# Performance work log

Hardware: AMD Instinct MI355X
Metric: run time of the kernel (lower is better)

Reference implementation:

```python
import jax, jax.numpy as jnp
import numpy as np

FEATURES = 1024
NUM_HEADS = 16
HEAD_SIZE = FEATURES // NUM_HEADS
B, T = 4, 2048
LN_EPS = 1e-6


def setup_inputs() -> dict:
    key = jax.random.key(0)
    ks = jax.random.split(key, 12)
    C, H, D = FEATURES, NUM_HEADS, HEAD_SIZE
    s_in = 1.0 / np.sqrt(C)
    s_ff = 1.0 / np.sqrt(4 * C)
    return {
        "x": jax.random.normal(ks[0], (B, T, C), jnp.float32),
        # per-head Q/K/V projections (no bias), stacked over heads
        "wq": jax.random.normal(ks[1], (H, C, D), jnp.float32) * s_in,
        "wk": jax.random.normal(ks[2], (H, C, D), jnp.float32) * s_in,
        "wv": jax.random.normal(ks[3], (H, C, D), jnp.float32) * s_in,
        "w_proj": jax.random.normal(ks[4], (C, C), jnp.float32) * s_in,
        "b_proj": jnp.zeros((C,), jnp.float32),
        "w_ff1": jax.random.normal(ks[5], (C, 4 * C), jnp.float32) * s_in,
        "b_ff1": jnp.zeros((4 * C,), jnp.float32),
        "w_ff2": jax.random.normal(ks[6], (4 * C, C), jnp.float32) * s_ff,
        "b_ff2": jnp.zeros((C,), jnp.float32),
        "ln1_scale": jnp.ones((C,), jnp.float32),
        "ln1_bias": jnp.zeros((C,), jnp.float32),
        "ln2_scale": jnp.ones((C,), jnp.float32),
        "ln2_bias": jnp.zeros((C,), jnp.float32),
    }


def _layernorm(x, scale, bias):
    mu = jnp.mean(x, axis=-1, keepdims=True)
    var = jnp.mean(jnp.square(x - mu), axis=-1, keepdims=True)
    return (x - mu) * jax.lax.rsqrt(var + LN_EPS) * scale + bias


def reference(x, wq, wk, wv, w_proj, b_proj, w_ff1, b_ff1, w_ff2, b_ff2,
              ln1_scale, ln1_bias, ln2_scale, ln2_bias):
    Bn, Tn, C = x.shape
    res = x
    xn = _layernorm(x, ln1_scale, ln1_bias)
    # per-head projections, vectorized over heads: [B,H,T,D]
    q = jnp.einsum('btc,hcd->bhtd', xn, wq)
    k = jnp.einsum('btc,hcd->bhtd', xn, wk)
    v = jnp.einsum('btc,hcd->bhtd', xn, wv)
    wei = jnp.einsum('bhtd,bhsd->bhts', q, k)
    tril = jnp.tril(jnp.ones((Tn, Tn), jnp.float32))
    # NOTE: original scales by C**-0.5 (full feature dim, not head_size),
    # and multiplies after masking (-inf * scale stays -inf).
    wei = jnp.where(tril == 0, -jnp.inf, wei) * (C ** -0.5)
    wei = jax.nn.softmax(wei, axis=-1)
    out = jnp.einsum('bhts,bhsd->bhtd', wei, v)
    # concat heads back to [B,T,C]
    out = out.transpose(0, 2, 1, 3).reshape(Bn, Tn, C)
    x = res + out @ w_proj + b_proj
    res = x
    xn = _layernorm(x, ln2_scale, ln2_bias)
    h = jax.nn.relu(xn @ w_ff1 + b_ff1)
    out = res + h @ w_ff2 + b_ff2
    return out
```

## Files before the change

kernel.cpp:

```cpp
#include <hip/hip_runtime.h>

#define Bn 4
#define Tn 2048
#define Cn 1024
#define Hn 16
#define Dn 64
#define Mr (Bn*Tn)

typedef _Float16 half8 __attribute__((ext_vector_type(8)));
typedef _Float16 half4v __attribute__((ext_vector_type(4)));
typedef float f32x4 __attribute__((ext_vector_type(4)));

__device__ __forceinline__ void g2l16(const void* g, void* l) {
  __builtin_amdgcn_global_load_lds((__attribute__((address_space(1))) void*)g,
                                   (__attribute__((address_space(3))) void*)l, 16, 0, 0);
}

__global__ __launch_bounds__(256) void transpose_f32_f16(const float* __restrict__ in,
                                                         _Float16* __restrict__ out,
                                                         int R, int C) {
  __shared__ float tile[32][33];
  const size_t zoff = (size_t)blockIdx.z * R * C;
  in += zoff; out += zoff;
  const int c0 = blockIdx.x * 32, r0 = blockIdx.y * 32;
  const int tx = threadIdx.x, ty = threadIdx.y;
#pragma unroll
  for (int i = 0; i < 4; ++i)
    tile[ty + i*8][tx] = in[(size_t)(r0 + ty + i*8) * C + c0 + tx];
  __syncthreads();
#pragma unroll
  for (int i = 0; i < 4; ++i)
    out[(size_t)(c0 + ty + i*8) * R + r0 + tx] = (_Float16)tile[tx][ty + i*8];
}

__global__ __launch_bounds__(256) void ln_row(const float* __restrict__ x,
                                              const float* __restrict__ g,
                                              const float* __restrict__ bta,
                                              _Float16* __restrict__ out) {
  const int row = blockIdx.x;
  const float4 v = ((const float4*)(x + (size_t)row * Cn))[threadIdx.x];
  float s  = v.x + v.y + v.z + v.w;
  float ss = v.x*v.x + v.y*v.y + v.z*v.z + v.w*v.w;
#pragma unroll
  for (int m = 1; m < 64; m <<= 1) { s += __shfl_xor(s, m); ss += __shfl_xor(ss, m); }
  __shared__ float red[8];
  const int wave = threadIdx.x >> 6, lane = threadIdx.x & 63;
  if (lane == 0) { red[wave] = s; red[4 + wave] = ss; }
  __syncthreads();
  s  = red[0] + red[1] + red[2] + red[3];
  ss = red[4] + red[5] + red[6] + red[7];
  const float mean = s * (1.0f/Cn);
  const float var  = ss * (1.0f/Cn) - mean*mean;
  const float rstd = rsqrtf(var + 1e-6f);
  const int c = threadIdx.x * 4;
  const float4 gg = ((const float4*)g)[threadIdx.x];
  const float4 bb = ((const float4*)bta)[threadIdx.x];
  half4v o;
  o[0] = (_Float16)((v.x - mean) * rstd * gg.x + bb.x);
  o[1] = (_Float16)((v.y - mean) * rstd * gg.y + bb.y);
  o[2] = (_Float16)((v.z - mean) * rstd * gg.z + bb.z);
  o[3] = (_Float16)((v.w - mean) * rstd * gg.w + bb.w);
  *((half4v*)(out + (size_t)row * Cn + c)) = o;
}

enum { EPI_QK = 0, EPI_V = 1, EPI_PROJ = 2, EPI_FF1 = 3, EPI_FF2 = 4 };

template<int EPI>
__global__ __launch_bounds__(256) void gemm_bt(const _Float16* __restrict__ A,
                                               const _Float16* __restrict__ Bt,
                                               void* __restrict__ outp,
                                               const float* __restrict__ bias,
                                               const float* __restrict__ resid,
                                               int M, int N, int K) {
  __shared__ __align__(16) _Float16 As[128*64];
  __shared__ __align__(16) _Float16 Bs[128*64];
  const int tid = threadIdx.x, wave = tid >> 6, lane = tid & 63;
  const int lr = lane & 15, lg = lane >> 4;
  const int brow = blockIdx.y * 128, bcol = blockIdx.x * 128;
  const int wrow = (wave >> 1) * 64, wcol = (wave & 1) * 64;
  f32x4 acc[4][4] = {};

  for (int kt = 0; kt < K; kt += 64) {
#pragma unroll
    for (int i = 0; i < 4; ++i) {
      const int chunk = i*4 + wave;
      const int e = chunk*512 + lane*8;
      const int rr = e >> 6, cc = e & 63;
      g2l16(A  + (size_t)(brow + rr)*K + kt + cc, As + chunk*512);
      g2l16(Bt + (size_t)(bcol + rr)*K + kt + cc, Bs + chunk*512);
    }
    __syncthreads();
#pragma unroll
    for (int kk = 0; kk < 64; kk += 32) {
      half8 af[4], bfr[4];
#pragma unroll
      for (int i = 0; i < 4; ++i) af[i]  = *(const half8*)(As + (wrow + i*16 + lr)*64 + kk + lg*8);
#pragma unroll
      for (int j = 0; j < 4; ++j) bfr[j] = *(const half8*)(Bs + (wcol + j*16 + lr)*64 + kk + lg*8);
#pragma unroll
      for (int i = 0; i < 4; ++i)
#pragma unroll
        for (int j = 0; j < 4; ++j)
          acc[i][j] = __builtin_amdgcn_mfma_f32_16x16x32_f16(af[i], bfr[j], acc[i][j], 0, 0, 0);
    }
    __syncthreads();
  }

  const int r0 = brow + wrow + lg*4;
  const int c0 = bcol + wcol + lr;
#pragma unroll
  for (int i = 0; i < 4; ++i) {
#pragma unroll
    for (int j = 0; j < 4; ++j) {
      const int col = c0 + j*16;
#pragma unroll
      for (int r = 0; r < 4; ++r) {
        const int row = r0 + i*16 + r;
        const float v = acc[i][j][r];
        if constexpr (EPI == EPI_QK) {
          ((_Float16*)outp)[(((size_t)(row >> 11) * Hn + (col >> 6)) * Tn + (row & 2047)) * Dn + (col & 63)] = (_Float16)v;
        } else if constexpr (EPI == EPI_V) {
          ((_Float16*)outp)[(((size_t)(row >> 11) * Hn + (col >> 6)) * Dn + (col & 63)) * Tn + (row & 2047)] = (_Float16)v;
        } else if constexpr (EPI == EPI_PROJ || EPI == EPI_FF2) {
          ((float*)outp)[(size_t)row * N + col] = v + bias[col] + resid[(size_t)row * N + col];
        } else if constexpr (EPI == EPI_FF1) {
          const float t = v + bias[col];
          ((_Float16*)outp)[(size_t)row * N + col] = (_Float16)(t > 0.f ? t : 0.f);
        }
      }
    }
  }
}

__global__ __launch_bounds__(256) void attn_kernel(const _Float16* __restrict__ q,
                                                   const _Float16* __restrict__ k,
                                                   const _Float16* __restrict__ vt,
                                                   _Float16* __restrict__ out) {
  const int qt = (int)(gridDim.x - 1 - blockIdx.x) * 128;
  const int h = blockIdx.y, b = blockIdx.z;
  const int tid = threadIdx.x, wave = tid >> 6, lane = tid & 63;
  const int lr = lane & 15, lg = lane >> 4;
  const size_t bh = (size_t)b * Hn + h;
  const _Float16* qg = q  + bh * (Tn * Dn);
  const _Float16* kg = k  + bh * (Tn * Dn);
  const _Float16* vg = vt + bh * (Dn * Tn);

  __shared__ __align__(16) _Float16 Ks[64*64];
  __shared__ __align__(16) _Float16 Vs[64*64];
  __shared__ __align__(16) _Float16 Ps[4][32*64];

  half8 qf[2][2];
#pragma unroll
  for (int i = 0; i < 2; ++i)
#pragma unroll
    for (int dh = 0; dh < 2; ++dh)
      qf[i][dh] = *(const half8*)(qg + (size_t)(qt + wave*32 + i*16 + lr)*Dn + dh*32 + lg*8);

  f32x4 oacc[2][4] = {};
  float mrow[2][4], lsum[2][4];
#pragma unroll
  for (int qi = 0; qi < 2; ++qi)
#pragma unroll
    for (int r = 0; r < 4; ++r) { mrow[qi][r] = -__builtin_inff(); lsum[qi][r] = 0.f; }

  const int qmax = qt + wave*32 + 31;

  for (int kvt = 0; kvt < qt + 128; kvt += 64) {
#pragma unroll
    for (int i = 0; i < 2; ++i) {
      const int chunk = i*4 + wave;
      const int e = chunk*512 + lane*8;
      const int rr = e >> 6, cc = e & 63;
      g2l16(kg + (size_t)(kvt + rr)*Dn + cc, Ks + chunk*512);
      g2l16(vg + (size_t)rr*Tn + kvt + cc,   Vs + chunk*512);
    }
    __syncthreads();

    if (kvt <= qmax) {
      half8 kb[4][2];
#pragma unroll
      for (int kv = 0; kv < 4; ++kv)
#pragma unroll
        for (int dh = 0; dh < 2; ++dh)
          kb[kv][dh] = *(const half8*)(Ks + (kv*16 + lr)*64 + dh*32 + lg*8);
      f32x4 sv[2][4];
#pragma unroll
      for (int qi = 0; qi < 2; ++qi)
#pragma unroll
        for (int kv = 0; kv < 4; ++kv) {
          f32x4 t = {0.f, 0.f, 0.f, 0.f};
          t = __builtin_amdgcn_mfma_f32_16x16x32_f16(qf[qi][0], kb[kv][0], t, 0, 0, 0);
          t = __builtin_amdgcn_mfma_f32_16x16x32_f16(qf[qi][1], kb[kv][1], t, 0, 0, 0);
          sv[qi][kv] = t;
        }
      const int qrow0 = qt + wave*32 + lg*4;
#pragma unroll
      for (int qi = 0; qi < 2; ++qi)
#pragma unroll
        for (int kv = 0; kv < 4; ++kv)
#pragma unroll
          for (int r = 0; r < 4; ++r) {
            const int qrow = qrow0 + qi*16 + r;
            const int kcol = kvt + kv*16 + lr;
            const float val = sv[qi][kv][r] * 0.03125f;
            sv[qi][kv][r] = (kcol > qrow) ? -__builtin_inff() : val;
          }
#pragma unroll
      for (int qi = 0; qi < 2; ++qi) {
        float tm[4], al[4], mn[4], ps[4];
#pragma unroll
        for (int r = 0; r < 4; ++r)
          tm[r] = fmaxf(fmaxf(sv[qi][0][r], sv[qi][1][r]), fmaxf(sv[qi][2][r], sv[qi][3][r]));
#pragma unroll
        for (int m = 1; m < 16; m <<= 1)
#pragma unroll
          for (int r = 0; r < 4; ++r)
            tm[r] = fmaxf(tm[r], __shfl_xor(tm[r], m));
#pragma unroll
        for (int r = 0; r < 4; ++r) {
          mn[r] = fmaxf(mrow[qi][r], tm[r]);
          al[r] = __expf(mrow[qi][r] - mn[r]);
          mrow[qi][r] = mn[r];
          ps[r] = 0.f;
        }
#pragma unroll
        for (int kv = 0; kv < 4; ++kv)
#pragma unroll
          for (int r = 0; r < 4; ++r) {
            const float p = __expf(sv[qi][kv][r] - mn[r]);
            ps[r] += p;
            Ps[wave][(qi*16 + lg*4 + r)*64 + kv*16 + lr] = (_Float16)p;
          }
#pragma unroll
        for (int m = 1; m < 16; m <<= 1)
#pragma unroll
          for (int r = 0; r < 4; ++r)
            ps[r] += __shfl_xor(ps[r], m);
#pragma unroll
        for (int r = 0; r < 4; ++r)
          lsum[qi][r] = lsum[qi][r]*al[r] + ps[r];
#pragma unroll
        for (int df = 0; df < 4; ++df)
#pragma unroll
          for (int r = 0; r < 4; ++r)
            oacc[qi][df][r] *= al[r];
      }
      half8 vb[4][2];
#pragma unroll
      for (int df = 0; df < 4; ++df)
#pragma unroll
        for (int kh = 0; kh < 2; ++kh)
          vb[df][kh] = *(const half8*)(Vs + (df*16 + lr)*64 + kh*32 + lg*8);
#pragma unroll
      for (int qi = 0; qi < 2; ++qi) {
        half8 pa[2];
#pragma unroll
        for (int kh = 0; kh < 2; ++kh)
          pa[kh] = *(const half8*)(&Ps[wave][(qi*16 + lr)*64 + kh*32 + lg*8]);
#pragma unroll
        for (int df = 0; df < 4; ++df) {
          oacc[qi][df] = __builtin_amdgcn_mfma_f32_16x16x32_f16(pa[0], vb[df][0], oacc[qi][df], 0, 0, 0);
          oacc[qi][df] = __builtin_amdgcn_mfma_f32_16x16x32_f16(pa[1], vb[df][1], oacc[qi][df], 0, 0, 0);
        }
      }
    }
    __syncthreads();
  }

#pragma unroll
  for (int qi = 0; qi < 2; ++qi)
#pragma unroll
    for (int df = 0; df < 4; ++df)
#pragma unroll
      for (int r = 0; r < 4; ++r) {
        const int row = qt + wave*32 + qi*16 + lg*4 + r;
        const int col = h*Dn + df*16 + lr;
        const float o = oacc[qi][df][r] / lsum[qi][r];
        out[((size_t)b*Tn + row)*Cn + col] = (_Float16)o;
      }
}

extern "C" void kernel_launch(void* const* d_in, const int* in_sizes, int n_in,
                              void* d_out, int out_size, void* d_ws, size_t ws_size,
                              hipStream_t stream) {
  const float* x      = (const float*)d_in[0];
  const float* wq     = (const float*)d_in[1];
  const float* wk     = (const float*)d_in[2];
  const float* wv     = (const float*)d_in[3];
  const float* w_proj = (const float*)d_in[4];
  const float* b_proj = (const float*)d_in[5];
  const float* w_ff1  = (const float*)d_in[6];
  const float* b_ff1  = (const float*)d_in[7];
  const float* w_ff2  = (const float*)d_in[8];
  const float* b_ff2  = (const float*)d_in[9];
  const float* ln1s   = (const float*)d_in[10];
  const float* ln1b   = (const float*)d_in[11];
  const float* ln2s   = (const float*)d_in[12];
  const float* ln2b   = (const float*)d_in[13];
  float* outp = (float*)d_out;

  char* ws = (char*)d_ws;
  constexpr size_t MB = (size_t)1 << 20;
  _Float16* Wq_t  = (_Float16*)(ws + 0*MB);
  _Float16* Wk_t  = (_Float16*)(ws + 2*MB);
  _Float16* Wv_t  = (_Float16*)(ws + 4*MB);
  _Float16* Wp_t  = (_Float16*)(ws + 6*MB);
  _Float16* Wf1_t = (_Float16*)(ws + 8*MB);
  _Float16* Wf2_t = (_Float16*)(ws + 16*MB);
  _Float16* xn    = (_Float16*)(ws + 24*MB);
  _Float16* attn_o= (_Float16*)(ws + 24*MB);
  _Float16* qbuf  = (_Float16*)(ws + 40*MB);
  _Float16* kbuf  = (_Float16*)(ws + 56*MB);
  _Float16* vtbuf = (_Float16*)(ws + 72*MB);
  _Float16* hbuf  = (_Float16*)(ws + 40*MB);
  float*    x2    = (float*)   (ws + 104*MB);
  _Float16* xn2   = (_Float16*)(ws + 136*MB);

  dim3 tb(32, 8);
  transpose_f32_f16<<<dim3(2, 32, 16), tb, 0, stream>>>(wq, Wq_t, 1024, 64);
  transpose_f32_f16<<<dim3(2, 32, 16), tb, 0, stream>>>(wk, Wk_t, 1024, 64);
  transpose_f32_f16<<<dim3(2, 32, 16), tb, 0, stream>>>(wv, Wv_t, 1024, 64);
  transpose_f32_f16<<<dim3(32, 32, 1), tb, 0, stream>>>(w_proj, Wp_t, 1024, 1024);
  transpose_f32_f16<<<dim3(128, 32, 1), tb, 0, stream>>>(w_ff1, Wf1_t, 1024, 4096);
  transpose_f32_f16<<<dim3(32, 128, 1), tb, 0, stream>>>(w_ff2, Wf2_t, 4096, 1024);

  ln_row<<<Mr, 256, 0, stream>>>(x, ln1s, ln1b, xn);

  gemm_bt<EPI_QK><<<dim3(8, 64), 256, 0, stream>>>(xn, Wq_t, qbuf, nullptr, nullptr, Mr, Cn, Cn);
  gemm_bt<EPI_QK><<<dim3(8, 64), 256, 0, stream>>>(xn, Wk_t, kbuf, nullptr, nullptr, Mr, Cn, Cn);
  gemm_bt<EPI_V ><<<dim3(8, 64), 256, 0, stream>>>(xn, Wv_t, vtbuf, nullptr, nullptr, Mr, Cn, Cn);

  attn_kernel<<<dim3(Tn/128, Hn, Bn), 256, 0, stream>>>(qbuf, kbuf, vtbuf, attn_o);

  gemm_bt<EPI_PROJ><<<dim3(8, 64), 256, 0, stream>>>(attn_o, Wp_t, x2, b_proj, x, Mr, Cn, Cn);

  ln_row<<<Mr, 256, 0, stream>>>(x2, ln2s, ln2b, xn2);

  gemm_bt<EPI_FF1><<<dim3(32, 64), 256, 0, stream>>>(xn2, Wf1_t, hbuf, b_ff1, nullptr, Mr, 4*Cn, Cn);
  gemm_bt<EPI_FF2><<<dim3(8, 64), 256, 0, stream>>>(hbuf, Wf2_t, outp, b_ff2, x2, Mr, Cn, 4*Cn);
}
```

Baseline: 719.8 us.

## Double-buffer K/V tiles, swizzle LDS, and keep softmax probabilities in registers

Rewrites the attention kernel. The next K/V tile is prefetched into a second LDS buffer while the current one is computed, and the LDS layout is XOR-swizzled to avoid bank conflicts. S is now computed as K·Q^T, so each lane owns one query row; this makes the row max and sum need only two cross-lane shuffles, and P is rebuilt into MFMA A-operand layout with shuffles instead of a round trip through LDS. The changes add shuffle work and register pressure, and they rely on the single end-of-loop barrier being enough to protect the buffer being overwritten.

```diff
diff --git a/kernel.cpp b/kernel.cpp
--- a/kernel.cpp
+++ b/kernel.cpp
@@ -10,6 +10,7 @@
 typedef _Float16 half8 __attribute__((ext_vector_type(8)));
 typedef _Float16 half4v __attribute__((ext_vector_type(4)));
 typedef float f32x4 __attribute__((ext_vector_type(4)));
+typedef unsigned u32x4 __attribute__((ext_vector_type(4)));
 
 __device__ __forceinline__ void g2l16(const void* g, void* l) {
   __builtin_amdgcn_global_load_lds((__attribute__((address_space(1))) void*)g,
@@ -145,122 +146,135 @@
   const _Float16* kg = k  + bh * (Tn * Dn);
   const _Float16* vg = vt + bh * (Dn * Tn);
 
-  __shared__ __align__(16) _Float16 Ks[64*64];
-  __shared__ __align__(16) _Float16 Vs[64*64];
-  __shared__ __align__(16) _Float16 Ps[4][32*64];
+  __shared__ __align__(16) _Float16 Ks[2][64*64];
+  __shared__ __align__(16) _Float16 Vs[2][64*64];
 
   half8 qf[2][2];
 #pragma unroll
-  for (int i = 0; i < 2; ++i)
+  for (int qi = 0; qi < 2; ++qi)
 #pragma unroll
     for (int dh = 0; dh < 2; ++dh)
-      qf[i][dh] = *(const half8*)(qg + (size_t)(qt + wave*32 + i*16 + lr)*Dn + dh*32 + lg*8);
+      qf[qi][dh] = *(const half8*)(qg + (size_t)(qt + wave*32 + qi*16 + lr)*Dn + dh*32 + lg*8);
 
   f32x4 oacc[2][4] = {};
-  float mrow[2][4], lsum[2][4];
-#pragma unroll
-  for (int qi = 0; qi < 2; ++qi)
-#pragma unroll
-    for (int r = 0; r < 4; ++r) { mrow[qi][r] = -__builtin_inff(); lsum[qi][r] = 0.f; }
+  float mrow[2] = {-__builtin_inff(), -__builtin_inff()};
+  float lsum[2] = {0.f, 0.f};
 
   const int qmax = qt + wave*32 + 31;
-
-  for (int kvt = 0; kvt < qt + 128; kvt += 64) {
-#pragma unroll
-    for (int i = 0; i < 2; ++i) {
-      const int chunk = i*4 + wave;
-      const int e = chunk*512 + lane*8;
-      const int rr = e >> 6, cc = e & 63;
-      g2l16(kg + (size_t)(kvt + rr)*Dn + cc, Ks + chunk*512);
-      g2l16(vg + (size_t)rr*Tn + kvt + cc,   Vs + chunk*512);
-    }
-    __syncthreads();
+  const int nt = (qt + 128) >> 6;
+
+  auto STAGE = [&](int bufi, int t) {
+    const int kvt = t * 64;
+#pragma unroll
+    for (int r = 0; r < 2; ++r) {
+      const int g0 = r*256 + wave*64;
+      const int g  = g0 + lane;
+      const int rr = g >> 3;
+      const int cs = (g & 7) ^ (rr & 7);
+      g2l16(kg + (size_t)(kvt + rr)*Dn + cs*8, &Ks[bufi][g0*8]);
+      g2l16(vg + (size_t)rr*Tn + kvt + cs*8,   &Vs[bufi][g0*8]);
+    }
+  };
+
+  STAGE(0, 0);
+  __syncthreads();
+
+  for (int t = 0; t < nt; ++t) {
+    const int kvt = t * 64;
+    if (t + 1 < nt) STAGE((t + 1) & 1, t + 1);
 
     if (kvt <= qmax) {
+      const _Float16* KS = Ks[t & 1];
+      const _Float16* VS = Vs[t & 1];
       half8 kb[4][2];
 #pragma unroll
-      for (int kv = 0; kv < 4; ++kv)
+      for (int f = 0; f < 4; ++f)
 #pragma unroll
         for (int dh = 0; dh < 2; ++dh)
-          kb[kv][dh] = *(const half8*)(Ks + (kv*16 + lr)*64 + dh*32 + lg*8);
-      f32x4 sv[2][4];
-#pragma unroll
-      for (int qi = 0; qi < 2; ++qi)
-#pragma unroll
-        for (int kv = 0; kv < 4; ++kv) {
-          f32x4 t = {0.f, 0.f, 0.f, 0.f};
-          t = __builtin_amdgcn_mfma_f32_16x16x32_f16(qf[qi][0], kb[kv][0], t, 0, 0, 0);
-          t = __builtin_amdgcn_mfma_f32_16x16x32_f16(qf[qi][1], kb[kv][1], t, 0, 0, 0);
-          sv[qi][kv] = t;
+          kb[f][dh] = *(const half8*)(KS + (16*f + lr)*64 + (((4*dh + lg) ^ (lr & 7)) * 8));
+
+#pragma unroll
+      for (int qi = 0; qi < 2; ++qi) {
+        f32x4 sv[4];
+#pragma unroll
+        for (int f = 0; f < 4; ++f) {
+          f32x4 tacc = {0.f, 0.f, 0.f, 0.f};
+          tacc = __builtin_amdgcn_mfma_f32_16x16x32_f16(kb[f][0], qf[qi][0], tacc, 0, 0, 0);
+          tacc = __builtin_amdgcn_mfma_f32_16x16x32_f16(kb[f][1], qf[qi][1], tacc, 0, 0, 0);
+          sv[f] = tacc;
         }
-      const int qrow0 = qt + wave*32 + lg*4;
-#pragma unroll
-      for (int qi = 0; qi < 2; ++qi)
-#pragma unroll
-        for (int kv = 0; kv < 4; ++kv)
+        const int qrow = qt + wave*32 + qi*16 + lr;
+#pragma unroll
+        for (int f = 0; f < 4; ++f)
 #pragma unroll
           for (int r = 0; r < 4; ++r) {
-            const int qrow = qrow0 + qi*16 + r;
-            const int kcol = kvt + kv*16 + lr;
-            const float val = sv[qi][kv][r] * 0.03125f;
-            sv[qi][kv][r] = (kcol > qrow) ? -__builtin_inff() : val;
+            const int kvv = kvt + 16*f + 4*lg + r;
+            sv[f][r] = (kvv > qrow) ? -__builtin_inff() : sv[f][r] * 0.03125f;
           }
-#pragma unroll
-      for (int qi = 0; qi < 2; ++qi) {
-        float tm[4], al[4], mn[4], ps[4];
-#pragma unroll
-        for (int r = 0; r < 4; ++r)
-          tm[r] = fmaxf(fmaxf(sv[qi][0][r], sv[qi][1][r]), fmaxf(sv[qi][2][r], sv[qi][3][r]));
-#pragma unroll
-        for (int m = 1; m < 16; m <<= 1)
-#pragma unroll
-          for (int r = 0; r < 4; ++r)
-            tm[r] = fmaxf(tm[r], __shfl_xor(tm[r], m));
-#pragma unroll
-        for (int r = 0; r < 4; ++r) {
-          mn[r] = fmaxf(mrow[qi][r], tm[r]);
-          al[r] = __expf(mrow[qi][r] - mn[r]);
-          mrow[qi][r] = mn[r];
-          ps[r] = 0.f;
+        float tm = sv[0][0];
+#pragma unroll
+        for (int f = 0; f < 4; ++f)
+#pragma unroll
+          for (int r = 0; r < 4; ++r) tm = fmaxf(tm, sv[f][r]);
+        tm = fmaxf(tm, __shfl_xor(tm, 16));
+        tm = fmaxf(tm, __shfl_xor(tm, 32));
+        const float mn = fmaxf(mrow[qi], tm);
+        const float alpha = __expf(mrow[qi] - mn);
+        mrow[qi] = mn;
+        float ps = 0.f;
+#pragma unroll
+        for (int f = 0; f < 4; ++f)
+#pragma unroll
+          for (int r = 0; r < 4; ++r) {
+            const float e = __expf(sv[f][r] - mn);
+            ps += e;
+            sv[f][r] = e;
+          }
+        ps += __shfl_xor(ps, 16);
+        ps += __shfl_xor(ps, 32);
+        lsum[qi] = lsum[qi] * alpha + ps;
+        unsigned ph[4][2];
+#pragma unroll
+        for (int f = 0; f < 4; ++f)
+#pragma unroll
+          for (int m = 0; m < 2; ++m) {
+            const unsigned lo = (unsigned)__builtin_bit_cast(unsigned short, (_Float16)sv[f][2*m]);
+            const unsigned hi = (unsigned)__builtin_bit_cast(unsigned short, (_Float16)sv[f][2*m + 1]);
+            ph[f][m] = lo | (hi << 16);
+          }
+        float ab[4];
+#pragma unroll
+        for (int r = 0; r < 4; ++r) ab[r] = __shfl(alpha, 4*lg + r);
+#pragma unroll
+        for (int df = 0; df < 4; ++df)
+#pragma unroll
+          for (int r = 0; r < 4; ++r) oacc[qi][df][r] *= ab[r];
+        const int s0 = lr + 16*(2*(lg & 1));
+        const int s1 = s0 + 16;
+        half8 pa[2];
+#pragma unroll
+        for (int kh = 0; kh < 2; ++kh) {
+          u32x4 w = {0u, 0u, 0u, 0u};
+#pragma unroll
+          for (int fi = 0; fi < 2; ++fi) {
+            const unsigned a0 = __shfl(ph[2*kh + fi][0], s0);
+            const unsigned a1 = __shfl(ph[2*kh + fi][1], s0);
+            const unsigned a2 = __shfl(ph[2*kh + fi][0], s1);
+            const unsigned a3 = __shfl(ph[2*kh + fi][1], s1);
+            const bool sel = ((lg >> 1) == fi);
+            w[0] = sel ? a0 : w[0];
+            w[1] = sel ? a1 : w[1];
+            w[2] = sel ? a2 : w[2];
+            w[3] = sel ? a3 : w[3];
+          }
+          pa[kh] = __builtin_bit_cast(half8, w);
         }
 #pragma unroll
-        for (int kv = 0; kv < 4; ++kv)
-#pragma unroll
-          for (int r = 0; r < 4; ++r) {
-            const float p = __expf(sv[qi][kv][r] - mn[r]);
-            ps[r] += p;
-            Ps[wave][(qi*16 + lg*4 + r)*64 + kv*16 + lr] = (_Float16)p;
-          }
-#pragma unroll
-        for (int m = 1; m < 16; m <<= 1)
-#pragma unroll
-          for (int r = 0; r < 4; ++r)
-            ps[r] += __shfl_xor(ps[r], m);
-#pragma unroll
-        for (int r = 0; r < 4; ++r)
-          lsum[qi][r] = lsum[qi][r]*al[r] + ps[r];
-#pragma unroll
-        for (int df = 0; df < 4; ++df)
-#pragma unroll
-          for (int r = 0; r < 4; ++r)
-            oacc[qi][df][r] *= al[r];
-      }
-      half8 vb[4][2];
-#pragma unroll
-      for (int df = 0; df < 4; ++df)
-#pragma unroll
-        for (int kh = 0; kh < 2; ++kh)
-          vb[df][kh] = *(const half8*)(Vs + (df*16 + lr)*64 + kh*32 + lg*8);
-#pragma unroll
-      for (int qi = 0; qi < 2; ++qi) {
-        half8 pa[2];
-#pragma unroll
-        for (int kh = 0; kh < 2; ++kh)
-          pa[kh] = *(const half8*)(&Ps[wave][(qi*16 + lr)*64 + kh*32 + lg*8]);
-#pragma unroll
         for (int df = 0; df < 4; ++df) {
-          oacc[qi][df] = __builtin_amdgcn_mfma_f32_16x16x32_f16(pa[0], vb[df][0], oacc[qi][df], 0, 0, 0);
-          oacc[qi][df] = __builtin_amdgcn_mfma_f32_16x16x32_f16(pa[1], vb[df][1], oacc[qi][df], 0, 0, 0);
+          half8 vb0 = *(const half8*)(VS + (16*df + lr)*64 + (((0 + lg) ^ (lr & 7)) * 8));
+          half8 vb1 = *(const half8*)(VS + (16*df + lr)*64 + (((4 + lg) ^ (lr & 7)) * 8));
+          oacc[qi][df] = __builtin_amdgcn_mfma_f32_16x16x32_f16(pa[0], vb0, oacc[qi][df], 0, 0, 0);
+          oacc[qi][df] = __builtin_amdgcn_mfma_f32_16x16x32_f16(pa[1], vb1, oacc[qi][df], 0, 0, 0);
         }
       }
     }
@@ -268,16 +282,20 @@
   }
 
 #pragma unroll
-  for (int qi = 0; qi < 2; ++qi)
+  for (int qi = 0; qi < 2; ++qi) {
+    const float linv = 1.0f / lsum[qi];
+    float lb[4];
+#pragma unroll
+    for (int r = 0; r < 4; ++r) lb[r] = __shfl(linv, 4*lg + r);
 #pragma unroll
     for (int df = 0; df < 4; ++df)
 #pragma unroll
       for (int r = 0; r < 4; ++r) {
-        const int row = qt + wave*32 + qi*16 + lg*4 + r;
+        const int row = qt + wave*32 + qi*16 + 4*lg + r;
         const int col = h*Dn + df*16 + lr;
-        const float o = oacc[qi][df][r] / lsum[qi][r];
-        out[((size_t)b*Tn + row)*Cn + col] = (_Float16)o;
+        out[((size_t)b*Tn + row)*Cn + col] = (_Float16)(oacc[qi][df][r] * lb[r]);
       }
+  }
 }
 
 extern "C" void kernel_launch(void* const* d_in, const int* in_sizes, int n_in,
@@ -289,8 +307,8 @@
   const float* wv     = (const float*)d_in[3];
   const float* w_proj = (const float*)d_in[4];
   const float* b_proj = (const float*)d_in[5];
+  const float* b_ff1  = (const float*)d_in[7];
   const float* w_ff1  = (const float*)d_in[6];
-  const float* b_ff1  = (const float*)d_in[7];
   const float* w_ff2  = (const float*)d_in[8];
   const float* b_ff2  = (const float*)d_in[9];
   const float* ln1s   = (const float*)d_in[10];
```

Result: faster. 663.6 us (-7.8%).
